# Kernel optimization log

Measured on AMD Instinct MI355X. Metric: run time of the kernel, lower is better.

Reference implementation:

```python
import jax, jax.numpy as jnp
import numpy as np


def setup_inputs() -> dict:
    key = jax.random.key(0)
    vel = jax.random.normal(key, (10000, 1000, 3), dtype=jnp.float32)
    return {"vel": vel, "vacf_window": 100}


def reference(vel, vacf_window):
    # vel: [T, N, 3]; output: [vacf_window]
    T = vel.shape[0]
    flat = vel.reshape(T, -1)  # [T, N*3]
    # lag 0: mean(vel * vel)
    terms = [jnp.mean(flat * flat)]
    # lags 1..vacf_window-1: mean over (T - t) * N * 3 elements
    for t in range(1, vacf_window):
        terms.append(jnp.mean(flat[t:] * flat[:-t]))
    return jnp.stack(terms)
```

## Files before the change

kernel.cpp:

```cpp
#include <hip/hip_runtime.h>


#define T_DIM 10000
#define C_DIM 3000
#define W 100
#define MA 112
#define NA 7
#define SROWS 224
#define NBB 90
#define KSPLIT 24
#define CPB 4
#define KB 32
#define LPAD 34
#define NPART 8

typedef __attribute__((ext_vector_type(8))) short short8;
typedef __attribute__((ext_vector_type(4))) short short4v;
typedef __attribute__((ext_vector_type(4))) float float4v;

__device__ __forceinline__ short f2bf(float f) {
    unsigned u = __float_as_uint(f);
    u += 0x7fffu + ((u >> 16) & 1u);
    return (short)(u >> 16);
}

__global__ __launch_bounds__(256, 8)
void vacf_mfma(const float* __restrict__ X, float* __restrict__ partial) {
    const int tid  = threadIdx.x;
    const int lane = tid & 63;
    const int wv   = tid >> 6;
    const int xcd  = blockIdx.x & 7;
    const int j    = blockIdx.x >> 3;
    const int ksix = xcd + 8 * (j / NBB);
    const int bb   = j % NBB;
    const int i0   = bb * MA;
    const int ks   = ksix * (CPB * KB);
    const int ke   = (ks + CPB * KB < C_DIM) ? (ks + CPB * KB) : C_DIM;
    const int nit  = (ke - ks + KB - 1) / KB;

    __shared__ short buf[SROWS * LPAD];
    __shared__ float bins[W];
    if (tid < W) bins[tid] = 0.f;

    const int cp = tid & 7;
    const int r0 = tid >> 3;

    const int n    = lane & 15;
    const int quad = lane >> 4;
    const int d0   = 2 * wv;
    const short* fragbase = &buf[n * LPAD + quad * 8];

    float4v acc0 = {0.f, 0.f, 0.f, 0.f};
    float4v acc1 = {0.f, 0.f, 0.f, 0.f};
    float4v pf[NA];

    {
        const int k0 = ks;
        #pragma unroll
        for (int s = 0; s < NA; ++s) {
            const int row = i0 + r0 + 32 * s;
            const int col = k0 + 4 * cp;
            if (row < T_DIM) {
                pf[s] = *(const float4v*)(X + (size_t)row * C_DIM + col);
            } else {
                pf[s] = (float4v){0.f, 0.f, 0.f, 0.f};
            }
        }
    }

    #pragma unroll 1
    for (int it = 0; it < nit; ++it) {
        __syncthreads();

        #pragma unroll
        for (int s = 0; s < NA; ++s) {
            short4v o;
            o[0] = f2bf(pf[s][0]); o[1] = f2bf(pf[s][1]);
            o[2] = f2bf(pf[s][2]); o[3] = f2bf(pf[s][3]);
            *(short4v*)&buf[(r0 + 32 * s) * LPAD + 4 * cp] = o;
        }
        __syncthreads();

        if (it + 1 < nit) {
            const int k0 = ks + (it + 1) * KB;
            const bool kfull = (k0 + KB <= ke);
            #pragma unroll
            for (int s = 0; s < NA; ++s) {
                const int row = i0 + r0 + 32 * s;
                const int col = k0 + 4 * cp;
                if ((row < T_DIM) & kfull) {
                    pf[s] = *(const float4v*)(X + (size_t)row * C_DIM + col);
                } else {
                    #pragma unroll
                    for (int e = 0; e < 4; ++e)
                        pf[s][e] = (row < T_DIM && col + e < ke)
                                     ? X[(size_t)row * C_DIM + col + e] : 0.f;
                }
            }
        }

        short8 fa[NA], fb[8];
        #pragma unroll
        for (int a = 0; a < NA; ++a)
            fa[a] = *(const short8*)(fragbase + 16 * a * LPAD);
        #pragma unroll
        for (int u = 0; u < 8; ++u)
            fb[u] = *(const short8*)(fragbase + 16 * (d0 + u) * LPAD);

        #pragma unroll
        for (int a = 0; a < NA; ++a) {
            acc0 = __builtin_amdgcn_mfma_f32_16x16x32_bf16(fa[a], fb[a],     acc0, 0, 0, 0);
            acc1 = __builtin_amdgcn_mfma_f32_16x16x32_bf16(fa[a], fb[a + 1], acc1, 0, 0, 0);
        }
    }

    #pragma unroll
    for (int p = 0; p < 4; ++p) {
        const int m  = quad * 4 + p;
        const int t0 = 16 * d0 + n - m;
        if (t0 >= 0 && t0 < W) atomicAdd(&bins[t0], acc0[p]);
        const int t1 = t0 + 16;
        if (t1 >= 0 && t1 < W) atomicAdd(&bins[t1], acc1[p]);
    }
    __syncthreads();
    if (tid < W) atomicAdd(&partial[xcd * W + tid], bins[tid]);
}

__global__ void vacf_scale(const float* __restrict__ partial, float* __restrict__ out) {
    int t = threadIdx.x;
    if (t < W) {
        float s = 0.f;
        #pragma unroll
        for (int b = 0; b < NPART; ++b) s += partial[b * W + t];
        out[t] = s / ((float)(T_DIM - t) * (float)C_DIM);
    }
}

extern "C" void kernel_launch(void* const* d_in, const int* in_sizes, int n_in,
                              void* d_out, int out_size, void* d_ws, size_t ws_size,
                              hipStream_t stream) {
    const float* X = (const float*)d_in[0];
    float* out = (float*)d_out;
    float* ws  = (float*)d_ws;

    hipMemsetAsync(ws, 0, NPART * W * sizeof(float), stream);
    vacf_mfma<<<NBB * KSPLIT, 256, 0, stream>>>(X, ws);
    vacf_scale<<<1, 128, 0, stream>>>(ws, out);
}
```

Before: 229.0 us.

## Stage fp32 tiles into double-buffered LDS via global_load_lds with swizzle

After: 214.2 us. 1.07x faster.

```diff
diff --git a/kernel.cpp b/kernel.cpp
--- a/kernel.cpp
+++ b/kernel.cpp
@@ -13,6 +13,7 @@
 #define KB 32
 #define LPAD 34
 #define NPART 8
+#define BUFB (SROWS * KB * 4)
 
 typedef __attribute__((ext_vector_type(8))) short short8;
 typedef __attribute__((ext_vector_type(4))) short short4v;
@@ -24,7 +25,23 @@
     return (short)(u >> 16);
 }
 
-__global__ __launch_bounds__(256, 8)
+__device__ __forceinline__ void gload_lds16(const float* src, char* dst) {
+    __builtin_amdgcn_global_load_lds(
+        (const __attribute__((address_space(1))) float*)src,
+        (__attribute__((address_space(3))) float*)dst, 16, 0, 0);
+}
+
+__device__ __forceinline__ short8 ldfrag(const char* lbase, int row, int q) {
+    const int off = row * 128 + ((q * 32) ^ ((row & 7) << 4));
+    const float4v u0 = *(const float4v*)(lbase + off);
+    const float4v u1 = *(const float4v*)(lbase + (off ^ 16));
+    short8 r;
+    r[0] = f2bf(u0[0]); r[1] = f2bf(u0[1]); r[2] = f2bf(u0[2]); r[3] = f2bf(u0[3]);
+    r[4] = f2bf(u1[0]); r[5] = f2bf(u1[1]); r[6] = f2bf(u1[2]); r[7] = f2bf(u1[3]);
+    return r;
+}
+
+__global__ __launch_bounds__(256, 2)
 void vacf_mfma(const float* __restrict__ X, float* __restrict__ partial) {
     const int tid  = threadIdx.x;
     const int lane = tid & 63;
@@ -35,83 +52,136 @@
     const int bb   = j % NBB;
     const int i0   = bb * MA;
     const int ks   = ksix * (CPB * KB);
-    const int ke   = (ks + CPB * KB < C_DIM) ? (ks + CPB * KB) : C_DIM;
-    const int nit  = (ke - ks + KB - 1) / KB;
-
-    __shared__ short buf[SROWS * LPAD];
+
+    __shared__ __align__(16) char lds[2 * BUFB];
     __shared__ float bins[W];
     if (tid < W) bins[tid] = 0.f;
-
-    const int cp = tid & 7;
-    const int r0 = tid >> 3;
 
     const int n    = lane & 15;
     const int quad = lane >> 4;
     const int d0   = 2 * wv;
-    const short* fragbase = &buf[n * LPAD + quad * 8];
 
     float4v acc0 = {0.f, 0.f, 0.f, 0.f};
     float4v acc1 = {0.f, 0.f, 0.f, 0.f};
-    float4v pf[NA];
-
-    {
-        const int k0 = ks;
+
+    const bool fast = (i0 + SROWS <= T_DIM) && (ksix < KSPLIT - 1);
+
+    if (fast) {
+        const int lr = lane >> 3;
+        const int lg = lane & 7;
+
+        #define STAGE(bi, k0)                                                    \
+            {                                                                    \
+                char* lb = lds + (bi) * BUFB + 56 * wv * 128;                    \
+                _Pragma("unroll")                                                \
+                for (int m = 0; m < 7; ++m) {                                    \
+                    const int rl = 56 * wv + 8 * m + lr;                         \
+                    const float* src = X + (size_t)(i0 + rl) * C_DIM + (k0)      \
+                                         + 4 * (lg ^ (rl & 7));                  \
+                    gload_lds16(src, lb + m * 1024);                             \
+                }                                                                \
+            }
+
+        STAGE(0, ks)
+
         #pragma unroll
-        for (int s = 0; s < NA; ++s) {
-            const int row = i0 + r0 + 32 * s;
-            const int col = k0 + 4 * cp;
-            if (row < T_DIM) {
-                pf[s] = *(const float4v*)(X + (size_t)row * C_DIM + col);
+        for (int it = 0; it < CPB; ++it) {
+            const int cur = it & 1;
+            if (it + 1 < CPB) {
+                STAGE(cur ^ 1, ks + (it + 1) * KB)
+                asm volatile("s_waitcnt vmcnt(7)" ::: "memory");
             } else {
-                pf[s] = (float4v){0.f, 0.f, 0.f, 0.f};
-            }
+                asm volatile("s_waitcnt vmcnt(0)" ::: "memory");
+            }
+            __builtin_amdgcn_s_barrier();
+
+            const char* lbase = lds + cur * BUFB;
+            short8 fa[NA], fb[8];
+            #pragma unroll
+            for (int a = 0; a < NA; ++a)
+                fa[a] = ldfrag(lbase, 16 * a + n, quad);
+            #pragma unroll
+            for (int u = 0; u < 8; ++u)
+                fb[u] = ldfrag(lbase, 16 * (d0 + u) + n, quad);
+
+            #pragma unroll
+            for (int a = 0; a < NA; ++a) {
+                acc0 = __builtin_amdgcn_mfma_f32_16x16x32_bf16(fa[a], fb[a],     acc0, 0, 0, 0);
+                acc1 = __builtin_amdgcn_mfma_f32_16x16x32_bf16(fa[a], fb[a + 1], acc1, 0, 0, 0);
+            }
+
+            __builtin_amdgcn_sched_barrier(0);
+            __builtin_amdgcn_s_barrier();
         }
-    }
-
-    #pragma unroll 1
-    for (int it = 0; it < nit; ++it) {
-        __syncthreads();
-
-        #pragma unroll
-        for (int s = 0; s < NA; ++s) {
-            short4v o;
-            o[0] = f2bf(pf[s][0]); o[1] = f2bf(pf[s][1]);
-            o[2] = f2bf(pf[s][2]); o[3] = f2bf(pf[s][3]);
-            *(short4v*)&buf[(r0 + 32 * s) * LPAD + 4 * cp] = o;
-        }
-        __syncthreads();
-
-        if (it + 1 < nit) {
-            const int k0 = ks + (it + 1) * KB;
-            const bool kfull = (k0 + KB <= ke);
+        #undef STAGE
+    } else {
+        short* buf = (short*)lds;
+        const int ke  = (ks + CPB * KB < C_DIM) ? (ks + CPB * KB) : C_DIM;
+        const int nit = (ke - ks + KB - 1) / KB;
+        const int cp  = tid & 7;
+        const int r0  = tid >> 3;
+        const short* fragbase = &buf[n * LPAD + quad * 8];
+        float4v pf[NA];
+
+        {
+            const int k0 = ks;
             #pragma unroll
             for (int s = 0; s < NA; ++s) {
                 const int row = i0 + r0 + 32 * s;
                 const int col = k0 + 4 * cp;
-                if ((row < T_DIM) & kfull) {
+                if (row < T_DIM) {
                     pf[s] = *(const float4v*)(X + (size_t)row * C_DIM + col);
                 } else {
-                    #pragma unroll
-                    for (int e = 0; e < 4; ++e)
-                        pf[s][e] = (row < T_DIM && col + e < ke)
-                                     ? X[(size_t)row * C_DIM + col + e] : 0.f;
+                    pf[s] = (float4v){0.f, 0.f, 0.f, 0.f};
                 }
             }
         }
 
-        short8 fa[NA], fb[8];
-        #pragma unroll
-        for (int a = 0; a < NA; ++a)
-            fa[a] = *(const short8*)(fragbase + 16 * a * LPAD);
-        #pragma unroll
-        for (int u = 0; u < 8; ++u)
-            fb[u] = *(const short8*)(fragbase + 16 * (d0 + u) * LPAD);
-
-        #pragma unroll
-        for (int a = 0; a < NA; ++a) {
-            acc0 = __builtin_amdgcn_mfma_f32_16x16x32_bf16(fa[a], fb[a],     acc0, 0, 0, 0);
-            acc1 = __builtin_amdgcn_mfma_f32_16x16x32_bf16(fa[a], fb[a + 1], acc1, 0, 0, 0);
+        #pragma unroll 1
+        for (int it = 0; it < nit; ++it) {
+            __syncthreads();
+            #pragma unroll
+            for (int s = 0; s < NA; ++s) {
+                short4v o;
+                o[0] = f2bf(pf[s][0]); o[1] = f2bf(pf[s][1]);
+                o[2] = f2bf(pf[s][2]); o[3] = f2bf(pf[s][3]);
+                *(short4v*)&buf[(r0 + 32 * s) * LPAD + 4 * cp] = o;
+            }
+            __syncthreads();
+
+            if (it + 1 < nit) {
+                const int k0 = ks + (it + 1) * KB;
+                const bool kfull = (k0 + KB <= ke);
+                #pragma unroll
+                for (int s = 0; s < NA; ++s) {
+                    const int row = i0 + r0 + 32 * s;
+                    const int col = k0 + 4 * cp;
+                    if ((row < T_DIM) & kfull) {
+                        pf[s] = *(const float4v*)(X + (size_t)row * C_DIM + col);
+                    } else {
+                        #pragma unroll
+                        for (int e = 0; e < 4; ++e)
+                            pf[s][e] = (row < T_DIM && col + e < ke)
+                                         ? X[(size_t)row * C_DIM + col + e] : 0.f;
+                    }
+                }
+            }
+
+            short8 fa[NA], fb[8];
+            #pragma unroll
+            for (int a = 0; a < NA; ++a)
+                fa[a] = *(const short8*)(fragbase + 16 * a * LPAD);
+            #pragma unroll
+            for (int u = 0; u < 8; ++u)
+                fb[u] = *(const short8*)(fragbase + 16 * (d0 + u) * LPAD);
+
+            #pragma unroll
+            for (int a = 0; a < NA; ++a) {
+                acc0 = __builtin_amdgcn_mfma_f32_16x16x32_bf16(fa[a], fb[a],     acc0, 0, 0, 0);
+                acc1 = __builtin_amdgcn_mfma_f32_16x16x32_bf16(fa[a], fb[a + 1], acc1, 0, 0, 0);
+            }
         }
+        __syncthreads();
     }
 
     #pragma unroll
```

## Pre-convert input to swizzled bf16 chunk layout and stream via LDS-direct loads

Applied to the files above, without the earlier changes.

Result: faster. 210.9 us (-7.9%).

```diff
diff --git a/kernel.cpp b/kernel.cpp
--- a/kernel.cpp
+++ b/kernel.cpp
@@ -4,19 +4,35 @@
 #define T_DIM 10000
 #define C_DIM 3000
 #define W 100
-#define MA 112
-#define NA 7
-#define SROWS 224
-#define NBB 90
-#define KSPLIT 24
-#define CPB 4
-#define KB 32
-#define LPAD 34
+
+#define CHUNKS 96
+#define RPAD 10368
+#define GRAN 64
+#define YOFF 4096
+#define WS_NEED (YOFF + (size_t)CHUNKS * RPAD * GRAN)
+
+#define MA 256
+#define NA 16
+#define SROWS 384
+#define NBB 40
+#define KSPLIT 16
+#define CPB 6
+#define TILEB (SROWS * GRAN)
 #define NPART 8
+
+#define FB_MA 112
+#define FB_NA 7
+#define FB_SROWS 224
+#define FB_NBB 90
+#define FB_KSPLIT 24
+#define FB_CPB 4
+#define FB_KB 32
+#define FB_LPAD 34
 
 typedef __attribute__((ext_vector_type(8))) short short8;
 typedef __attribute__((ext_vector_type(4))) short short4v;
 typedef __attribute__((ext_vector_type(4))) float float4v;
+typedef __attribute__((ext_vector_type(4))) unsigned int uint4v;
 
 __device__ __forceinline__ short f2bf(float f) {
     unsigned u = __float_as_uint(f);
@@ -24,8 +40,51 @@
     return (short)(u >> 16);
 }
 
-__global__ __launch_bounds__(256, 8)
-void vacf_mfma(const float* __restrict__ X, float* __restrict__ partial) {
+__device__ __forceinline__ void gload_lds16(const char* src, char* dst) {
+    __builtin_amdgcn_global_load_lds(
+        (const __attribute__((address_space(1))) unsigned int*)src,
+        (__attribute__((address_space(3))) unsigned int*)dst, 16, 0, 0);
+}
+
+__global__ __launch_bounds__(256)
+void vacf_relayout(const float* __restrict__ X, char* __restrict__ Y) {
+    __shared__ char tile[64 * 528];
+    const int tid = threadIdx.x;
+    const int bc  = blockIdx.x % 12;
+    const int br  = blockIdx.x / 12;
+    const int r0  = br * 64;
+    const int c0  = bc * 256;
+
+    #pragma unroll
+    for (int k = 0; k < 16; ++k) {
+        const int rl  = k * 4 + (tid >> 6);
+        const int col = (tid & 63) * 4;
+        const int row = r0 + rl;
+        float4v v = {0.f, 0.f, 0.f, 0.f};
+        if (row < T_DIM && c0 + col + 4 <= C_DIM)
+            v = *(const float4v*)(X + (size_t)row * C_DIM + c0 + col);
+        short4v o;
+        o[0] = f2bf(v[0]); o[1] = f2bf(v[1]); o[2] = f2bf(v[2]); o[3] = f2bf(v[3]);
+        const int cc = col >> 5, p = (col >> 3) & 3, sub = col & 7;
+        const int ps = p ^ ((rl >> 1) & 3);
+        *(short4v*)&tile[rl * 528 + cc * 64 + ps * 16 + sub * 2] = o;
+    }
+    __syncthreads();
+
+    #pragma unroll
+    for (int pass = 0; pass < 2; ++pass) {
+        const int g  = pass * 256 + tid;
+        const int cc = g >> 6, rl = g & 63;
+        char* dst = Y + ((size_t)(bc * 8 + cc) * RPAD + r0 + rl) * GRAN;
+        const char* s = &tile[rl * 528 + cc * 64];
+        #pragma unroll
+        for (int q = 0; q < 4; ++q)
+            *(uint4v*)(dst + q * 16) = *(const uint4v*)(s + q * 16);
+    }
+}
+
+__global__ __launch_bounds__(256, 3)
+void vacf_main(const char* __restrict__ Y, float* __restrict__ partial) {
     const int tid  = threadIdx.x;
     const int lane = tid & 63;
     const int wv   = tid >> 6;
@@ -34,58 +93,126 @@
     const int ksix = xcd + 8 * (j / NBB);
     const int bb   = j % NBB;
     const int i0   = bb * MA;
-    const int ks   = ksix * (CPB * KB);
-    const int ke   = (ks + CPB * KB < C_DIM) ? (ks + CPB * KB) : C_DIM;
-    const int nit  = (ke - ks + KB - 1) / KB;
-
-    __shared__ short buf[SROWS * LPAD];
+
+    __shared__ __align__(16) char lds[2 * TILEB];
     __shared__ float bins[W];
     if (tid < W) bins[tid] = 0.f;
-
-    const int cp = tid & 7;
-    const int r0 = tid >> 3;
 
     const int n    = lane & 15;
     const int quad = lane >> 4;
     const int d0   = 2 * wv;
-    const short* fragbase = &buf[n * LPAD + quad * 8];
+    const int fragoff = n * 64 + ((quad ^ ((n >> 1) & 3)) << 4);
+    const int lr16 = lane * 16;
 
     float4v acc0 = {0.f, 0.f, 0.f, 0.f};
     float4v acc1 = {0.f, 0.f, 0.f, 0.f};
-    float4v pf[NA];
+
+    #define STAGE(bi, cix)                                                     \
+        {                                                                      \
+            const char* sb = Y + ((size_t)(cix) * RPAD + i0 + wv * 96) * GRAN; \
+            char* db = lds + (bi) * TILEB + wv * 96 * GRAN;                    \
+            _Pragma("unroll")                                                  \
+            for (int m = 0; m < 6; ++m)                                        \
+                gload_lds16(sb + m * 1024 + lr16, db + m * 1024);              \
+        }
+
+    STAGE(0, ksix * CPB)
+
+    #pragma unroll
+    for (int it = 0; it < CPB; ++it) {
+        const int cur = it & 1;
+        if (it + 1 < CPB) {
+            STAGE(cur ^ 1, ksix * CPB + it + 1)
+            asm volatile("s_waitcnt vmcnt(6)" ::: "memory");
+        } else {
+            asm volatile("s_waitcnt vmcnt(0)" ::: "memory");
+        }
+        __builtin_amdgcn_s_barrier();
+
+        const char* lb = lds + cur * TILEB + fragoff;
+        short8 fbp = *(const short8*)(lb + d0 * 1024);
+        #pragma unroll
+        for (int a = 0; a < NA; ++a) {
+            const short8 fav = *(const short8*)(lb + a * 1024);
+            const short8 fbn = *(const short8*)(lb + (d0 + a + 1) * 1024);
+            acc0 = __builtin_amdgcn_mfma_f32_16x16x32_bf16(fav, fbp, acc0, 0, 0, 0);
+            acc1 = __builtin_amdgcn_mfma_f32_16x16x32_bf16(fav, fbn, acc1, 0, 0, 0);
+            fbp = fbn;
+        }
+
+        __builtin_amdgcn_sched_barrier(0);
+        __builtin_amdgcn_s_barrier();
+    }
+    #undef STAGE
+
+    #pragma unroll
+    for (int p = 0; p < 4; ++p) {
+        const int m  = quad * 4 + p;
+        const int t0 = 16 * d0 + n - m;
+        if (t0 >= 0 && t0 < W) atomicAdd(&bins[t0], acc0[p]);
+        const int t1 = t0 + 16;
+        if (t1 >= 0 && t1 < W) atomicAdd(&bins[t1], acc1[p]);
+    }
+    __syncthreads();
+    if (tid < W) atomicAdd(&partial[xcd * W + tid], bins[tid]);
+}
+
+__global__ __launch_bounds__(256, 2)
+void vacf_fb(const float* __restrict__ X, float* __restrict__ partial) {
+    const int tid  = threadIdx.x;
+    const int lane = tid & 63;
+    const int wv   = tid >> 6;
+    const int xcd  = blockIdx.x & 7;
+    const int j    = blockIdx.x >> 3;
+    const int ksix = xcd + 8 * (j / FB_NBB);
+    const int bb   = j % FB_NBB;
+    const int i0   = bb * FB_MA;
+    const int ks   = ksix * (FB_CPB * FB_KB);
+    const int ke   = (ks + FB_CPB * FB_KB < C_DIM) ? (ks + FB_CPB * FB_KB) : C_DIM;
+    const int nit  = (ke - ks + FB_KB - 1) / FB_KB;
+
+    __shared__ short buf[FB_SROWS * FB_LPAD];
+    __shared__ float bins[W];
+    if (tid < W) bins[tid] = 0.f;
+
+    const int cp = tid & 7;
+    const int r0 = tid >> 3;
+    const int n    = lane & 15;
+    const int quad = lane >> 4;
+    const int d0   = 2 * wv;
+    const short* fragbase = &buf[n * FB_LPAD + quad * 8];
+
+    float4v acc0 = {0.f, 0.f, 0.f, 0.f};
+    float4v acc1 = {0.f, 0.f, 0.f, 0.f};
+    float4v pf[FB_NA];
 
     {
-        const int k0 = ks;
-        #pragma unroll
-        for (int s = 0; s < NA; ++s) {
+        #pragma unroll
+        for (int s = 0; s < FB_NA; ++s) {
             const int row = i0 + r0 + 32 * s;
-            const int col = k0 + 4 * cp;
-            if (row < T_DIM) {
-                pf[s] = *(const float4v*)(X + (size_t)row * C_DIM + col);
-            } else {
-                pf[s] = (float4v){0.f, 0.f, 0.f, 0.f};
-            }
+            const int col = ks + 4 * cp;
+            pf[s] = (row < T_DIM) ? *(const float4v*)(X + (size_t)row * C_DIM + col)
+                                  : (float4v){0.f, 0.f, 0.f, 0.f};
         }
     }
 
     #pragma unroll 1
     for (int it = 0; it < nit; ++it) {
         __syncthreads();
-
-        #pragma unroll
-        for (int s = 0; s < NA; ++s) {
+        #pragma unroll
+        for (int s = 0; s < FB_NA; ++s) {
             short4v o;
             o[0] = f2bf(pf[s][0]); o[1] = f2bf(pf[s][1]);
             o[2] = f2bf(pf[s][2]); o[3] = f2bf(pf[s][3]);
-            *(short4v*)&buf[(r0 + 32 * s) * LPAD + 4 * cp] = o;
+            *(short4v*)&buf[(r0 + 32 * s) * FB_LPAD + 4 * cp] = o;
         }
         __syncthreads();
 
         if (it + 1 < nit) {
-            const int k0 = ks + (it + 1) * KB;
-            const bool kfull = (k0 + KB <= ke);
+            const int k0 = ks + (it + 1) * FB_KB;
+            const bool kfull = (k0 + FB_KB <= ke);
             #pragma unroll
-            for (int s = 0; s < NA; ++s) {
+            for (int s = 0; s < FB_NA; ++s) {
                 const int row = i0 + r0 + 32 * s;
                 const int col = k0 + 4 * cp;
                 if ((row < T_DIM) & kfull) {
@@ -99,16 +226,16 @@
             }
         }
 
-        short8 fa[NA], fb[8];
-        #pragma unroll
-        for (int a = 0; a < NA; ++a)
-            fa[a] = *(const short8*)(fragbase + 16 * a * LPAD);
+        short8 fa[FB_NA], fb[8];
+        #pragma unroll
+        for (int a = 0; a < FB_NA; ++a)
+            fa[a] = *(const short8*)(fragbase + 16 * a * FB_LPAD);
         #pragma unroll
         for (int u = 0; u < 8; ++u)
-            fb[u] = *(const short8*)(fragbase + 16 * (d0 + u) * LPAD);
-
-        #pragma unroll
-        for (int a = 0; a < NA; ++a) {
+            fb[u] = *(const short8*)(fragbase + 16 * (d0 + u) * FB_LPAD);
+
+        #pragma unroll
+        for (int a = 0; a < FB_NA; ++a) {
             acc0 = __builtin_amdgcn_mfma_f32_16x16x32_bf16(fa[a], fb[a],     acc0, 0, 0, 0);
             acc1 = __builtin_amdgcn_mfma_f32_16x16x32_bf16(fa[a], fb[a + 1], acc1, 0, 0, 0);
         }
@@ -144,6 +271,12 @@
     float* ws  = (float*)d_ws;
 
     hipMemsetAsync(ws, 0, NPART * W * sizeof(float), stream);
-    vacf_mfma<<<NBB * KSPLIT, 256, 0, stream>>>(X, ws);
+    if (ws_size >= WS_NEED) {
+        char* Y = (char*)d_ws + YOFF;
+        vacf_relayout<<<(RPAD / 64) * 12, 256, 0, stream>>>(X, Y);
+        vacf_main<<<NBB * KSPLIT, 256, 0, stream>>>(Y, ws);
+    } else {
+        vacf_fb<<<FB_NBB * FB_KSPLIT, 256, 0, stream>>>(X, ws);
+    }
     vacf_scale<<<1, 128, 0, stream>>>(ws, out);
 }
```

## Load whole 256-row, 64-column tile once into swizzled LDS and run MFMAs

Applied to the files above, without the earlier changes.

Result: faster. 186.7 us (-18.5%).

```diff
diff --git a/kernel.cpp b/kernel.cpp
--- a/kernel.cpp
+++ b/kernel.cpp
@@ -4,14 +4,12 @@
 #define T_DIM 10000
 #define C_DIM 3000
 #define W 100
-#define MA 112
-#define NA 7
-#define SROWS 224
-#define NBB 90
-#define KSPLIT 24
-#define CPB 4
-#define KB 32
-#define LPAD 34
+#define MA 256
+#define NA 16
+#define SROWS 384
+#define NBB 40
+#define KS 47
+#define KW 64
 #define NPART 8
 
 typedef __attribute__((ext_vector_type(8))) short short8;
@@ -24,93 +22,80 @@
     return (short)(u >> 16);
 }
 
-__global__ __launch_bounds__(256, 8)
-void vacf_mfma(const float* __restrict__ X, float* __restrict__ partial) {
+__global__ __launch_bounds__(256, 3)
+void vacf_fused(const float* __restrict__ X, float* __restrict__ partial) {
     const int tid  = threadIdx.x;
     const int lane = tid & 63;
     const int wv   = tid >> 6;
-    const int xcd  = blockIdx.x & 7;
-    const int j    = blockIdx.x >> 3;
-    const int ksix = xcd + 8 * (j / NBB);
-    const int bb   = j % NBB;
+    const int ksix = blockIdx.x % KS;
+    const int bb   = blockIdx.x / KS;
     const int i0   = bb * MA;
-    const int ks   = ksix * (CPB * KB);
-    const int ke   = (ks + CPB * KB < C_DIM) ? (ks + CPB * KB) : C_DIM;
-    const int nit  = (ke - ks + KB - 1) / KB;
+    const int c0   = ksix * KW;
 
-    __shared__ short buf[SROWS * LPAD];
+    __shared__ __align__(16) char lds[SROWS * 128];
     __shared__ float bins[W];
     if (tid < W) bins[tid] = 0.f;
 
-    const int cp = tid & 7;
-    const int r0 = tid >> 3;
+    const int rr = tid >> 4;
+    const int cl = (tid & 15) * 4;
+    const int sw = ((((cl >> 3) ^ (rr & 7)) << 4) | ((cl & 7) << 1));
+
+    const bool fast = (i0 + SROWS <= T_DIM) && (c0 + KW <= C_DIM);
+    if (fast) {
+        #pragma unroll
+        for (int b = 0; b < 3; ++b) {
+            float4v v[8];
+            #pragma unroll
+            for (int m = 0; m < 8; ++m) {
+                const int row = b * 128 + m * 16 + rr;
+                v[m] = *(const float4v*)(X + (size_t)(i0 + row) * C_DIM + c0 + cl);
+            }
+            #pragma unroll
+            for (int m = 0; m < 8; ++m) {
+                const int row = b * 128 + m * 16 + rr;
+                short4v o;
+                o[0] = f2bf(v[m][0]); o[1] = f2bf(v[m][1]);
+                o[2] = f2bf(v[m][2]); o[3] = f2bf(v[m][3]);
+                *(short4v*)&lds[row * 128 + sw] = o;
+            }
+        }
+    } else {
+        #pragma unroll
+        for (int b = 0; b < 3; ++b) {
+            #pragma unroll
+            for (int m = 0; m < 8; ++m) {
+                const int row = b * 128 + m * 16 + rr;
+                const int gr  = i0 + row;
+                float4v v = {0.f, 0.f, 0.f, 0.f};
+                if (gr < T_DIM && c0 + cl + 4 <= C_DIM)
+                    v = *(const float4v*)(X + (size_t)gr * C_DIM + c0 + cl);
+                short4v o;
+                o[0] = f2bf(v[0]); o[1] = f2bf(v[1]);
+                o[2] = f2bf(v[2]); o[3] = f2bf(v[3]);
+                *(short4v*)&lds[row * 128 + sw] = o;
+            }
+        }
+    }
+    __syncthreads();
 
     const int n    = lane & 15;
     const int quad = lane >> 4;
     const int d0   = 2 * wv;
-    const short* fragbase = &buf[n * LPAD + quad * 8];
 
     float4v acc0 = {0.f, 0.f, 0.f, 0.f};
     float4v acc1 = {0.f, 0.f, 0.f, 0.f};
-    float4v pf[NA];
 
-    {
-        const int k0 = ks;
-        #pragma unroll
-        for (int s = 0; s < NA; ++s) {
-            const int row = i0 + r0 + 32 * s;
-            const int col = k0 + 4 * cp;
-            if (row < T_DIM) {
-                pf[s] = *(const float4v*)(X + (size_t)row * C_DIM + col);
-            } else {
-                pf[s] = (float4v){0.f, 0.f, 0.f, 0.f};
-            }
-        }
-    }
-
-    #pragma unroll 1
-    for (int it = 0; it < nit; ++it) {
-        __syncthreads();
-
-        #pragma unroll
-        for (int s = 0; s < NA; ++s) {
-            short4v o;
-            o[0] = f2bf(pf[s][0]); o[1] = f2bf(pf[s][1]);
-            o[2] = f2bf(pf[s][2]); o[3] = f2bf(pf[s][3]);
-            *(short4v*)&buf[(r0 + 32 * s) * LPAD + 4 * cp] = o;
-        }
-        __syncthreads();
-
-        if (it + 1 < nit) {
-            const int k0 = ks + (it + 1) * KB;
-            const bool kfull = (k0 + KB <= ke);
-            #pragma unroll
-            for (int s = 0; s < NA; ++s) {
-                const int row = i0 + r0 + 32 * s;
-                const int col = k0 + 4 * cp;
-                if ((row < T_DIM) & kfull) {
-                    pf[s] = *(const float4v*)(X + (size_t)row * C_DIM + col);
-                } else {
-                    #pragma unroll
-                    for (int e = 0; e < 4; ++e)
-                        pf[s][e] = (row < T_DIM && col + e < ke)
-                                     ? X[(size_t)row * C_DIM + col + e] : 0.f;
-                }
-            }
-        }
-
-        short8 fa[NA], fb[8];
-        #pragma unroll
-        for (int a = 0; a < NA; ++a)
-            fa[a] = *(const short8*)(fragbase + 16 * a * LPAD);
-        #pragma unroll
-        for (int u = 0; u < 8; ++u)
-            fb[u] = *(const short8*)(fragbase + 16 * (d0 + u) * LPAD);
-
+    #pragma unroll
+    for (int kk = 0; kk < 2; ++kk) {
+        const char* lb = lds + n * 128 + (((((kk << 2) | quad)) ^ (n & 7)) << 4);
+        short8 fbp = *(const short8*)(lb + d0 * 2048);
         #pragma unroll
         for (int a = 0; a < NA; ++a) {
-            acc0 = __builtin_amdgcn_mfma_f32_16x16x32_bf16(fa[a], fb[a],     acc0, 0, 0, 0);
-            acc1 = __builtin_amdgcn_mfma_f32_16x16x32_bf16(fa[a], fb[a + 1], acc1, 0, 0, 0);
+            const short8 fav = *(const short8*)(lb + a * 2048);
+            const short8 fbn = *(const short8*)(lb + (d0 + a + 1) * 2048);
+            acc0 = __builtin_amdgcn_mfma_f32_16x16x32_bf16(fav, fbp, acc0, 0, 0, 0);
+            acc1 = __builtin_amdgcn_mfma_f32_16x16x32_bf16(fav, fbn, acc1, 0, 0, 0);
+            fbp = fbn;
         }
     }
 
@@ -123,7 +108,7 @@
         if (t1 >= 0 && t1 < W) atomicAdd(&bins[t1], acc1[p]);
     }
     __syncthreads();
-    if (tid < W) atomicAdd(&partial[xcd * W + tid], bins[tid]);
+    if (tid < W) atomicAdd(&partial[(blockIdx.x & 7) * W + tid], bins[tid]);
 }
 
 __global__ void vacf_scale(const float* __restrict__ partial, float* __restrict__ out) {
@@ -144,6 +129,6 @@
     float* ws  = (float*)d_ws;
 
     hipMemsetAsync(ws, 0, NPART * W * sizeof(float), stream);
-    vacf_mfma<<<NBB * KSPLIT, 256, 0, stream>>>(X, ws);
+    vacf_fused<<<NBB * KS, 256, 0, stream>>>(X, ws);
     vacf_scale<<<1, 128, 0, stream>>>(ws, out);
 }
```
